# Kernel tuning notes

Measured on AMD Instinct MI355X. Metric: run time of the kernel, lower is better.

Reference implementation:

```python
import jax, jax.numpy as jnp
import numpy as np

B, S, D = 2, 1024, 2048
H, DN, DR, DV, R = 16, 128, 64, 128, 512
E, K, FI, SI = 12, 4, 1408, 2816
THETA = 10000.0
EPS = 1e-6


def rmsnorm(x, w):
    return x * jax.lax.rsqrt(jnp.mean(x * x, -1, keepdims=True) + EPS) * w


def rope(x, cos, sin):
    # interleaved-pair rotation (torch view_as_complex convention)
    x1, x2 = x[..., 0::2], x[..., 1::2]
    return jnp.stack([x1 * cos - x2 * sin, x1 * sin + x2 * cos], axis=-1).reshape(x.shape)


def setup_inputs() -> dict:
    key = jax.random.key(0)
    ks = jax.random.split(key, 16)
    w = lambda k, sh: jax.random.normal(k, sh, jnp.float32) * 0.02
    inp = {
        'x': jax.random.normal(ks[0], (B, S, D), jnp.float32),
        'wq': w(ks[1], (D, H * (DN + DR))),
        'wkv_a': w(ks[2], (D, R + DR)),
        'kv_norm_w': jnp.ones((R,), jnp.float32),
        'wkv_b': w(ks[3], (R, H * (DN + DV))),
        'wo': w(ks[4], (H * DV, D)),
        'norm_w': jnp.ones((D,), jnp.float32),
        'gate_w': w(ks[5], (D, E)),
        'gate_b': jnp.zeros((E,), jnp.float32),
        'w1': w(ks[6], (E, D, FI)),
        'w2': w(ks[7], (E, FI, D)),
        'w3': w(ks[8], (E, D, FI)),
        'ws1': w(ks[9], (D, SI)),
        'ws2': w(ks[10], (SI, D)),
        'ws3': w(ks[11], (D, SI)),
        'mask': jnp.triu(jnp.full((S, S), -1e9, jnp.float32), 1),  # causal
        'start_pos': 0,
    }
    return inp


def reference(x, wq, wkv_a, kv_norm_w, wkv_b, wo, norm_w, gate_w, gate_b,
              w1, w2, w3, ws1, ws2, ws3, mask, start_pos):
    def mla(h):
        q = (h @ wq).reshape(B, S, H, DN + DR)
        q_nope, q_pe = q[..., :DN], q[..., DN:]
        kv = h @ wkv_a                              # [B,S,R+DR]
        kv_lat = rmsnorm(kv[..., :R], kv_norm_w)    # latent KV (kv_lora_rank)
        k_pe = kv[..., R:]                          # [B,S,DR] shared across heads
        kvb = (kv_lat @ wkv_b).reshape(B, S, H, DN + DV)
        k_nope, v = kvb[..., :DN], kvb[..., DN:]
        pos = start_pos + jnp.arange(S)
        inv = 1.0 / (THETA ** (jnp.arange(0, DR, 2, dtype=jnp.float32) / DR))
        ang = pos[:, None].astype(jnp.float32) * inv[None, :]
        cos, sin = jnp.cos(ang), jnp.sin(ang)       # [S, DR//2]
        q_pe = rope(q_pe, cos[None, :, None, :], sin[None, :, None, :])
        k_pe = rope(k_pe, cos[None, :, :], sin[None, :, :])
        scale = (DN + DR) ** -0.5
        scores = (jnp.einsum('bshd,bthd->bhst', q_nope, k_nope)
                  + jnp.einsum('bshd,btd->bhst', q_pe, k_pe)) * scale
        scores = scores + mask[None, None, :, :]
        p = jax.nn.softmax(scores, axis=-1)
        o = jnp.einsum('bhst,bthd->bshd', p, v).reshape(B, S, H * DV)
        return o @ wo

    def moe(h):
        t = h.reshape(-1, D)                        # [T, D]
        T = t.shape[0]
        s = jax.nn.sigmoid(t @ gate_w)              # routing scores [T, E]
        _, topi = jax.lax.top_k(s + gate_b[None, :], K)   # adaptive bias only for selection
        wgt = jnp.take_along_axis(s, topi, axis=1)
        wgt = wgt / jnp.sum(wgt, -1, keepdims=True)
        route = jnp.zeros((T, E), t.dtype).at[jnp.arange(T)[:, None], topi].set(wgt)
        hh = jnp.einsum('td,edi->eti', t, w1)
        gg = jax.nn.silu(hh) * jnp.einsum('td,edi->eti', t, w3)
        eo = jnp.einsum('eti,eid->etd', gg, w2)
        out = jnp.einsum('te,etd->td', route, eo)
        shared = (jax.nn.silu(t @ ws1) * (t @ ws3)) @ ws2
        return (out + shared).reshape(B, S, D)

    first = mla(rmsnorm(x, norm_w)) + x
    return moe(rmsnorm(first, norm_w)) + first
```

## Files before the change

### kernel.cpp

```cpp
#include <hip/hip_runtime.h>
#include <math.h>

typedef unsigned short u16;
typedef __attribute__((ext_vector_type(8))) short short8;
typedef __attribute__((ext_vector_type(8))) _Float16 half8;
typedef __attribute__((ext_vector_type(4))) float f32x4;

__device__ inline u16 f32_to_bf16_rne(float f){
    unsigned int u = __float_as_uint(f);
    unsigned int r = (u + 0x7FFFu + ((u >> 16) & 1u)) >> 16;
    return (u16)r;
}
__device__ inline float bf16_to_f32(u16 h){ return __uint_as_float(((unsigned int)h) << 16); }
__device__ inline u16 h2b(_Float16 h){ union { _Float16 f; u16 u; } x; x.f = h; return x.u; }

__device__ __forceinline__ void glds16(const void* g, void* l){
    __builtin_amdgcn_global_load_lds((const __attribute__((address_space(1))) void*)g,
                                     (__attribute__((address_space(3))) void*)l, 16, 0, 0);
}
#define WAIT_VM0()  { asm volatile("s_waitcnt vmcnt(0)" ::: "memory"); __builtin_amdgcn_sched_barrier(0); }
#define WAIT_VM3()  { asm volatile("s_waitcnt vmcnt(3)" ::: "memory"); __builtin_amdgcn_sched_barrier(0); }
#define WAIT_LGKM0() { asm volatile("s_waitcnt lgkmcnt(0)" ::: "memory"); __builtin_amdgcn_sched_barrier(0); }
#define RAW_BAR()   { __builtin_amdgcn_s_barrier(); __builtin_amdgcn_sched_barrier(0); }

#define TT 2048
#define DD 2048
#define SS 1024
#define NH 16

#define EPI_F32     0
#define EPI_BF16    1
#define EPI_RES     2
#define EPI_SILUMUL 3
#define EPI_F16PAIR 4
#define EPI_QROPE   5
#define EPI_QKV     6

template<int PAIR>
__global__ __launch_bounds__(256) void cvtT_k(const float* __restrict__ W, long long wstr,
        u16* __restrict__ WTh, u16* __restrict__ WTl, long long tstr, int K, int Nsrc){
    __shared__ float L[64][65];
    int e = blockIdx.z;
    const float* Wp = W + (long long)e * wstr;
    int k0 = blockIdx.y * 64, n0 = blockIdx.x * 64;
    int tid = threadIdx.x;
#pragma unroll
    for (int it = 0; it < 4; ++it) {
        int r = (tid >> 4) + it * 16, cc = (tid & 15) * 4;
        int col = n0 + cc;
        float4 v = {0.f, 0.f, 0.f, 0.f};
        if (col + 3 < Nsrc) v = *(const float4*)(Wp + (long long)(k0 + r) * Nsrc + col);
        else {
            const float* p = Wp + (long long)(k0 + r) * Nsrc;
            float tmp[4] = {0.f, 0.f, 0.f, 0.f};
#pragma unroll
            for (int q2 = 0; q2 < 4; q2++) if (col + q2 < Nsrc) tmp[q2] = p[col + q2];
            v.x = tmp[0]; v.y = tmp[1]; v.z = tmp[2]; v.w = tmp[3];
        }
        L[r][cc] = v.x; L[r][cc+1] = v.y; L[r][cc+2] = v.z; L[r][cc+3] = v.w;
    }
    __syncthreads();
#pragma unroll
    for (int it = 0; it < 2; ++it) {
        int idx = it * 256 + tid; int n = idx >> 3, kc = (idx & 7) * 8;
        u16 hi[8], lo[8];
#pragma unroll
        for (int u = 0; u < 8; ++u) {
            float v = L[kc + u][n];
            if (PAIR) { _Float16 h = (_Float16)v; hi[u] = h2b(h); lo[u] = h2b((_Float16)(v - (float)h)); }
            else hi[u] = f32_to_bf16_rne(v);
        }
        long long o = (long long)e * tstr + (long long)(n0 + n) * K + k0 + kc;
        *(short8*)(WTh + o) = *(short8*)hi;
        if (PAIR) *(short8*)(WTl + o) = *(short8*)lo;
    }
}

template<int EPI, bool PREC, bool AGLDS>
__global__ __launch_bounds__(256) void gemm_k(
    const u16* __restrict__ A0, const u16* __restrict__ A1, int lda,
    const u16* __restrict__ BTh, const u16* __restrict__ BTl, long long btstr,
    int M, int N, int K,
    const int* offs, const int* cnt, const int* gather, int ebase,
    void* C0, void* C1, int ldc,
    const void* aux, const float* __restrict__ cosT, const float* __restrict__ sinT,
    int zsplit)
{
    __shared__ u16 AsH[2][4096];
    __shared__ u16 AsL[PREC ? 2 : 1][PREC ? 4096 : 8];
    __shared__ u16 BsH[2][4096];
    __shared__ u16 BsL[PREC ? 2 : 1][PREC ? 4096 : 8];

    int tid  = threadIdx.x;
    int lane = tid & 63;
    int wv   = tid >> 6;
    int wm = (wv >> 1) * 64, wn = (wv & 1) * 64;

    int Lid = blockIdx.y * gridDim.x + blockIdx.x;
    int jj  = Lid >> 3;
    int yb  = jj % gridDim.y;
    int nb  = (Lid & 7) + ((jj / gridDim.y) << 3);
    int n0 = nb * 128;
    if (n0 >= N) return;

    int zz   = blockIdx.z;
    int e    = ebase + ((zsplit > 0 && zz >= zsplit) ? (zz - zsplit) : zz);
    int base = offs ? offs[e] : 0;
    int mc   = cnt ? cnt[e] : M;
    int m0   = yb * 128;
    if (m0 >= mc) return;
    const u16* Bh = BTh + (long long)zz * btstr;
    const u16* Bl = PREC ? (BTl + (long long)zz * btstr) : (const u16*)nullptr;
    void* Cw = (zsplit > 0 && zz >= zsplit) ? C1 : C0;

    int rr_ = tid >> 2, s4 = tid & 3;
    long long arow0 = -1, arow1 = -1;
    if (!AGLDS) {
        if (m0 + rr_ < mc)      arow0 = gather ? (long long)gather[base + m0 + rr_]      : (long long)(base + m0 + rr_);
        if (m0 + rr_ + 64 < mc) arow1 = gather ? (long long)gather[base + m0 + rr_ + 64] : (long long)(base + m0 + rr_ + 64);
    }

    f32x4 acc[4][4];
#pragma unroll
    for (int i = 0; i < 4; i++)
#pragma unroll
        for (int j = 0; j < 4; j++) { f32x4 z = {0.f,0.f,0.f,0.f}; acc[i][j] = z; }

    short8 zer = {0,0,0,0,0,0,0,0};
    short8 a0h = zer, a1h = zer, a0l = zer, a1l = zer;

    int gr0 = wv * 16 + (lane >> 2);
    int gsl = lane & 3;

#define STAGE_GL(PB, KT)                                                         \
    {                                                                            \
        _Pragma("unroll")                                                        \
        for (int it = 0; it < 2; ++it) {                                         \
            int r = it * 64 + gr0;                                               \
            int s = gsl ^ ((r >> 1) & 3);                                        \
            glds16(Bh + (long long)(n0 + r) * K + (KT) + s * 8,                  \
                   (char*)&BsH[PB][0] + it * 4096 + wv * 1024);                  \
            if (PREC)                                                            \
                glds16(Bl + (long long)(n0 + r) * K + (KT) + s * 8,              \
                       (char*)&BsL[PB][0] + it * 4096 + wv * 1024);              \
            if (AGLDS) {                                                         \
                glds16(A0 + (long long)(base + m0 + r) * lda + (KT) + s * 8,     \
                       (char*)&AsH[PB][0] + it * 4096 + wv * 1024);              \
                if (PREC)                                                        \
                    glds16(A1 + (long long)(base + m0 + r) * lda + (KT) + s * 8, \
                           (char*)&AsL[PB][0] + it * 4096 + wv * 1024);          \
            }                                                                    \
        }                                                                        \
        if (!AGLDS) {                                                            \
            a0h = (arow0 >= 0) ? *(const short8*)(A0 + arow0 * lda + (KT) + s4 * 8) : zer; \
            a1h = (arow1 >= 0) ? *(const short8*)(A0 + arow1 * lda + (KT) + s4 * 8) : zer; \
            if (PREC) {                                                          \
                a0l = (arow0 >= 0) ? *(const short8*)(A1 + arow0 * lda + (KT) + s4 * 8) : zer; \
                a1l = (arow1 >= 0) ? *(const short8*)(A1 + arow1 * lda + (KT) + s4 * 8) : zer; \
            }                                                                    \
        }                                                                        \
    }

    int pb = 0;
    STAGE_GL(0, 0);
    for (int kt = 0; kt < K; kt += 32) {
        WAIT_VM0();
        if (!AGLDS) {
            int d0 = rr_ * 64 + 16 * (s4 ^ ((rr_ >> 1) & 3));
            int r1w = rr_ + 64;
            int d1 = r1w * 64 + 16 * (s4 ^ ((r1w >> 1) & 3));
            *(short8*)((char*)&AsH[pb][0] + d0) = a0h;
            *(short8*)((char*)&AsH[pb][0] + d1) = a1h;
            if (PREC) {
                *(short8*)((char*)&AsL[pb][0] + d0) = a0l;
                *(short8*)((char*)&AsL[pb][0] + d1) = a1l;
            }
            WAIT_LGKM0();
        }
        RAW_BAR();
        if (kt + 32 < K) { STAGE_GL(pb ^ 1, kt + 32); }
        if (PREC) {
            half8 ah[4], al[4];
#pragma unroll
            for (int i = 0; i < 4; i++) {
                int ra = wm + i * 16 + (lane & 15);
                int off = ra * 64 + 16 * ((lane >> 4) ^ ((ra >> 1) & 3));
                ah[i] = *(const half8*)((const char*)&AsH[pb][0] + off);
                al[i] = *(const half8*)((const char*)&AsL[pb][0] + off);
            }
#pragma unroll
            for (int j = 0; j < 4; j++) {
                int rb = wn + j * 16 + (lane & 15);
                int off = rb * 64 + 16 * ((lane >> 4) ^ ((rb >> 1) & 3));
                half8 bh = *(const half8*)((const char*)&BsH[pb][0] + off);
                half8 bl = *(const half8*)((const char*)&BsL[pb][0] + off);
#pragma unroll
                for (int i = 0; i < 4; i++) {
                    acc[i][j] = __builtin_amdgcn_mfma_f32_16x16x32_f16(ah[i], bh, acc[i][j], 0, 0, 0);
                    acc[i][j] = __builtin_amdgcn_mfma_f32_16x16x32_f16(ah[i], bl, acc[i][j], 0, 0, 0);
                    acc[i][j] = __builtin_amdgcn_mfma_f32_16x16x32_f16(al[i], bh, acc[i][j], 0, 0, 0);
                }
            }
        } else {
            short8 af[4];
#pragma unroll
            for (int i = 0; i < 4; i++) {
                int ra = wm + i * 16 + (lane & 15);
                af[i] = *(const short8*)((const char*)&AsH[pb][0] + ra * 64 + 16 * ((lane >> 4) ^ ((ra >> 1) & 3)));
            }
#pragma unroll
            for (int j = 0; j < 4; j++) {
                int rb = wn + j * 16 + (lane & 15);
                short8 bfr = *(const short8*)((const char*)&BsH[pb][0] + rb * 64 + 16 * ((lane >> 4) ^ ((rb >> 1) & 3)));
#pragma unroll
                for (int i = 0; i < 4; i++)
                    acc[i][j] = __builtin_amdgcn_mfma_f32_16x16x32_bf16(af[i], bfr, acc[i][j], 0, 0, 0);
            }
        }
        pb ^= 1;
    }
#undef STAGE_GL

    if (EPI == EPI_QROPE || (EPI == EPI_QKV && n0 < 3072)) {
#pragma unroll
        for (int i = 0; i < 4; i++) {
            int rr0 = m0 + wm + i * 16 + ((lane >> 4) << 2);
#pragma unroll
            for (int j = 0; j < 4; j++) {
                int col = n0 + wn + j * 16 + (lane & 15);
                int hd = col % 192;
#pragma unroll
                for (int r = 0; r < 4; r++) {
                    int rr = rr0 + r;
                    float v = acc[i][j][r];
                    float pv = __shfl_xor(v, 1);
                    float outv = v;
                    if (hd >= 128) {
                        int s = rr & (SS - 1);
                        int pi2 = (hd - 128) >> 1;
                        float cc_ = cosT[s * 32 + pi2], sn_ = sinT[s * 32 + pi2];
                        bool odd = col & 1;
                        float a0 = odd ? pv : v, a1 = odd ? v : pv;
                        outv = odd ? (a0 * sn_ + a1 * cc_) : (a0 * cc_ - a1 * sn_);
                    }
                    long long cidx = (long long)rr * ldc + col;
                    _Float16 hh = (_Float16)outv;
                    ((u16*)C0)[cidx] = h2b(hh);
                    ((u16*)C1)[cidx] = h2b((_Float16)(outv - (float)hh));
                }
            }
        }
    } else if (EPI == EPI_QKV) {
        float* kvo = (float*)aux;
#pragma unroll
        for (int i = 0; i < 4; i++) {
            int rr0 = m0 + wm + i * 16 + ((lane >> 4) << 2);
#pragma unroll
            for (int j = 0; j < 4; j++) {
                int col = n0 + wn + j * 16 + (lane & 15);
                if (col >= 3648) continue;
#pragma unroll
                for (int r = 0; r < 4; r++) {
                    int rr = rr0 + r;
                    kvo[(long long)rr * 576 + (col - 3072)] = acc[i][j][r];
                }
            }
        }
    } else {
#pragma unroll
        for (int i = 0; i < 4; i++) {
            int rbase = m0 + wm + i * 16 + ((lane >> 4) << 2);
#pragma unroll
            for (int j = 0; j < 4; j++) {
                int col = n0 + wn + j * 16 + (lane & 15);
                if (col >= N) continue;
#pragma unroll
                for (int r = 0; r < 4; r++) {
                    int rr = rbase + r;
                    if (rr >= mc) continue;
                    long long cidx = (long long)(base + rr) * ldc + col;
                    float v = acc[i][j][r];
                    if (EPI == EPI_F32)      ((float*)C0)[cidx] = v;
                    else if (EPI == EPI_BF16) ((u16*)Cw)[cidx] = f32_to_bf16_rne(v);
                    else if (EPI == EPI_RES)  ((float*)C0)[cidx] = v + ((const float*)aux)[cidx];
                    else if (EPI == EPI_SILUMUL) {
                        float h1v = bf16_to_f32(((const u16*)aux)[cidx]);
                        float g = h1v / (1.f + __expf(-h1v)) * v;
                        ((u16*)C0)[cidx] = f32_to_bf16_rne(g);
                    } else {
                        _Float16 hh = (_Float16)v;
                        ((u16*)C0)[cidx] = h2b(hh);
                        ((u16*)C1)[cidx] = h2b((_Float16)(v - (float)hh));
                    }
                }
            }
        }
    }
}

template<int EPI, bool GATHER>
__global__ __launch_bounds__(256) void gemm3_k(
    const u16* __restrict__ A0, int lda,
    const u16* __restrict__ BTh, long long btstr,
    int M, int N, int K,
    const int* offs, const int* cnt, const int* gather, int ebase,
    void* C0, void* C1, int ldc,
    const void* aux, int zsplit)
{
    __shared__ u16 As[3][2048];
    __shared__ u16 Bs[3][4096];

    int tid  = threadIdx.x;
    int lane = tid & 63;
    int wv   = tid >> 6;
    int wm = (wv >> 1) * 32, wn = (wv & 1) * 64;

    int Lid = blockIdx.y * gridDim.x + blockIdx.x;
    int jj  = Lid >> 3;
    int yb  = jj % gridDim.y;
    int nb  = (Lid & 7) + ((jj / gridDim.y) << 3);
    int n0 = nb * 128;
    if (n0 >= N) return;

    int zz   = blockIdx.z;
    int e    = ebase + ((zsplit > 0 && zz >= zsplit) ? (zz - zsplit) : zz);
    int base = offs ? offs[e] : 0;
    int mc   = cnt ? cnt[e] : M;
    int m0   = yb * 64;
    if (m0 >= mc) return;
    const u16* Bh = BTh + (long long)zz * btstr;
    void* Cw = (zsplit > 0 && zz >= zsplit) ? C1 : C0;

    int rr = tid >> 2;
    int sl4 = tid & 3;
    int sA = sl4 ^ ((rr >> 1) & 3);
    long long bro0, bro1, aro0;
    {
        int rb1 = rr + 64;
        int sB1 = sl4 ^ ((rb1 >> 1) & 3);
        bro0 = (long long)(n0 + rr) * K + sA * 8;
        bro1 = (long long)(n0 + rb1) * K + sB1 * 8;
        int ar = m0 + rr; ar = (ar < mc) ? ar : (mc - 1);
        long long ga = GATHER ? (long long)gather[base + ar] : (long long)(base + ar);
        aro0 = ga * (long long)lda + sA * 8;
    }

    f32x4 acc[2][4];
#pragma unroll
    for (int i = 0; i < 2; i++)
#pragma unroll
        for (int j = 0; j < 4; j++) { f32x4 z = {0.f,0.f,0.f,0.f}; acc[i][j] = z; }

#define STG3(PB, KT)                                                        \
    {                                                                       \
        glds16(Bh + bro0 + (KT), (char*)&Bs[PB][0] + wv * 1024);            \
        glds16(Bh + bro1 + (KT), (char*)&Bs[PB][0] + 4096 + wv * 1024);     \
        glds16(A0 + aro0 + (KT), (char*)&As[PB][0] + wv * 1024);            \
    }

    int nst = K >> 5;
    STG3(0, 0);
    if (nst > 1) STG3(1, 32);
    for (int t = 0; t < nst; ++t) {
        if (t + 1 < nst) { WAIT_VM3(); }
        else            { WAIT_VM0(); }
        RAW_BAR();
        if (t + 2 < nst) { int p2 = (t + 2) % 3; STG3(p2, (t + 2) * 32); }
        int pb = t % 3;
        short8 af[2];
#pragma unroll
        for (int i = 0; i < 2; i++) {
            int ra = wm + i * 16 + (lane & 15);
            af[i] = *(const short8*)((const char*)&As[pb][0] + ra * 64 + 16 * ((lane >> 4) ^ ((ra >> 1) & 3)));
        }
#pragma unroll
        for (int j = 0; j < 4; j++) {
            int rb = wn + j * 16 + (lane & 15);
            short8 bfr = *(const short8*)((const char*)&Bs[pb][0] + rb * 64 + 16 * ((lane >> 4) ^ ((rb >> 1) & 3)));
#pragma unroll
            for (int i = 0; i < 2; i++)
                acc[i][j] = __builtin_amdgcn_mfma_f32_16x16x32_bf16(af[i], bfr, acc[i][j], 0, 0, 0);
        }
    }
#undef STG3

#pragma unroll
    for (int i = 0; i < 2; i++) {
        int rbase = m0 + wm + i * 16 + ((lane >> 4) << 2);
#pragma unroll
        for (int j = 0; j < 4; j++) {
            int col = n0 + wn + j * 16 + (lane & 15);
            if (col >= N) continue;
#pragma unroll
            for (int r = 0; r < 4; r++) {
                int rr2 = rbase + r;
                if (rr2 >= mc) continue;
                long long cidx = (long long)(base + rr2) * ldc + col;
                float v = acc[i][j][r];
                if (EPI == EPI_BF16) ((u16*)Cw)[cidx] = f32_to_bf16_rne(v);
                else {
                    float h1v = bf16_to_f32(((const u16*)aux)[cidx]);
                    float g = h1v / (1.f + __expf(-h1v)) * v;
                    ((u16*)C0)[cidx] = f32_to_bf16_rne(g);
                }
            }
        }
    }
}

__global__ __launch_bounds__(256) void silumul_k(u16* __restrict__ g, const u16* __restrict__ h3,
                                                 long long n){
    long long i = ((long long)blockIdx.x * 256 + threadIdx.x) * 8;
    if (i >= n) return;
    short8 a = *(const short8*)(g + i);
    short8 b = *(const short8*)(h3 + i);
    u16 o[8];
#pragma unroll
    for (int u = 0; u < 8; ++u) {
        float x = bf16_to_f32((u16)a[u]);
        float y = bf16_to_f32((u16)b[u]);
        o[u] = f32_to_bf16_rne(x / (1.f + __expf(-x)) * y);
    }
    *(short8*)(g + i) = *(short8*)o;
}

__global__ void costab_k(const int* sp, float* ct, float* st){
    int idx = blockIdx.x * 256 + threadIdx.x;
    if (idx >= SS * 32) return;
    int i = idx & 31, s = idx >> 5;
    float inv = powf(10000.0f, -(float)i / 32.0f);
    float a = (float)(sp[0] + s) * inv;
    ct[idx] = cosf(a);
    st[idx] = sinf(a);
}

template<int MODE>
__global__ __launch_bounds__(256) void rms_k(const float* __restrict__ x, const float* __restrict__ w,
                                             u16* o0, u16* o1){
    int t = blockIdx.x, tid = threadIdx.x;
    const float* row = x + (long long)t * DD;
    float4 v0 = *(const float4*)(row + tid * 4);
    float4 v1 = *(const float4*)(row + 1024 + tid * 4);
    float ss = v0.x*v0.x + v0.y*v0.y + v0.z*v0.z + v0.w*v0.w
             + v1.x*v1.x + v1.y*v1.y + v1.z*v1.z + v1.w*v1.w;
#pragma unroll
    for (int d = 1; d < 64; d <<= 1) ss += __shfl_xor(ss, d, 64);
    __shared__ float red[4];
    if ((tid & 63) == 0) red[tid >> 6] = ss;
    __syncthreads();
    float sc = rsqrtf((red[0] + red[1] + red[2] + red[3]) / (float)DD + 1e-6f);
    float a[8];
    a[0]=v0.x; a[1]=v0.y; a[2]=v0.z; a[3]=v0.w; a[4]=v1.x; a[5]=v1.y; a[6]=v1.z; a[7]=v1.w;
#pragma unroll
    for (int q2 = 0; q2 < 8; q2++) {
        int d = (q2 < 4) ? (tid * 4 + q2) : (1024 + tid * 4 + (q2 - 4));
        float y = a[q2] * sc * w[d];
        if (MODE == 0) {
            _Float16 hh = (_Float16)y;
            o0[(long long)t * DD + d] = h2b(hh);
            o1[(long long)t * DD + d] = h2b((_Float16)(y - (float)hh));
        } else {
            o0[(long long)t * DD + d] = f32_to_bf16_rne(y);
        }
    }
}

__global__ __launch_bounds__(256) void kvprep_k(const float* __restrict__ kv, const float* __restrict__ kw,
    const float* __restrict__ ct, const float* __restrict__ st,
    u16* lath, u16* latl, u16* kpeh, u16* kpel){
    int t = blockIdx.x, tid = threadIdx.x;
    const float* row = kv + (long long)t * 576;
    float x0 = row[tid], x1 = row[256 + tid];
    float ss = x0 * x0 + x1 * x1;
#pragma unroll
    for (int d = 1; d < 64; d <<= 1) ss += __shfl_xor(ss, d, 64);
    __shared__ float red[4];
    if ((tid & 63) == 0) red[tid >> 6] = ss;
    __syncthreads();
    float sc = rsqrtf((red[0] + red[1] + red[2] + red[3]) / 512.f + 1e-6f);
    float y0 = x0 * sc * kw[tid], y1 = x1 * sc * kw[256 + tid];
    _Float16 h0 = (_Float16)y0, h1 = (_Float16)y1;
    lath[(long long)t * 512 + tid] = h2b(h0);
    latl[(long long)t * 512 + tid] = h2b((_Float16)(y0 - (float)h0));
    lath[(long long)t * 512 + 256 + tid] = h2b(h1);
    latl[(long long)t * 512 + 256 + tid] = h2b((_Float16)(y1 - (float)h1));
    if (tid < 32) {
        int s = t & (SS - 1);
        float a0 = row[512 + 2 * tid], a1 = row[513 + 2 * tid];
        float c = ct[s * 32 + tid], sn = st[s * 32 + tid];
        float r0 = a0 * c - a1 * sn, r1 = a0 * sn + a1 * c;
        _Float16 p0 = (_Float16)r0, p1 = (_Float16)r1;
        kpeh[(long long)t * 64 + 2 * tid]     = h2b(p0);
        kpel[(long long)t * 64 + 2 * tid]     = h2b((_Float16)(r0 - (float)p0));
        kpeh[(long long)t * 64 + 2 * tid + 1] = h2b(p1);
        kpel[(long long)t * 64 + 2 * tid + 1] = h2b((_Float16)(r1 - (float)p1));
    }
}

__global__ __launch_bounds__(256) void vtprep_k(const u16* __restrict__ kvbh, const u16* __restrict__ kvbl,
                                                u16* vth, u16* vtl){
    __shared__ u16 L[64][136];
    int bh = blockIdx.x, st = blockIdx.y, pl = blockIdx.z;
    const u16* src = pl ? kvbl : kvbh;
    u16* dst = pl ? vtl : vth;
    int b = bh >> 4, hh = bh & 15;
    int tid = threadIdx.x;
#pragma unroll
    for (int it = 0; it < 4; ++it) {
        int idx = it * 256 + tid; int sl = idx >> 4, dc = idx & 15;
        long long t = (long long)b * SS + st * 64 + sl;
        *(short8*)&L[sl][dc * 8] = *(const short8*)(src + t * 4096 + hh * 256 + 128 + dc * 8);
    }
    __syncthreads();
#pragma unroll
    for (int it = 0; it < 4; ++it) {
        int idx = it * 256 + tid; int d = idx >> 3, sc = idx & 7;
        short8 v;
#pragma unroll
        for (int u = 0; u < 8; u++) v[u] = (short)L[sc * 8 + u][d];
        *(short8*)(dst + ((long long)bh * 128 + d) * SS + st * 64 + sc * 8) = v;
    }
}

__global__ __launch_bounds__(256) void attn_k(
    const u16* __restrict__ qh_, const u16* __restrict__ ql_,
    const u16* __restrict__ kvbh, const u16* __restrict__ kvbl,
    const u16* __restrict__ kpeh, const u16* __restrict__ kpel,
    const u16* __restrict__ vth, const u16* __restrict__ vtl,
    u16* ohi, u16* olo)
{
    __shared__ u16 KsH[32][200], KsL[32][200];
    __shared__ u16 VsH[128][40], VsL[128][40];
    __shared__ u16 PlH[4][16][40], PlL[4][16][40];
    int bx = blockIdx.x, bh = blockIdx.y;
    int qi = (bh & 16) ? bx : (15 - bx);
    int b = bh >> 4, h = bh & 15;
    int tid = threadIdx.x, lane = tid & 63, wv = tid >> 6;
    int q0 = qi * 64;
    const u16* vbh = vth + (long long)bh * 128 * SS;
    const u16* vbl = vtl + (long long)bh * 128 * SS;

    half8 qh[6], ql[6];
    {
        int row = q0 + wv * 16 + (lane & 15);
        const u16* ph = qh_ + (long long)(b * SS + row) * 3072 + h * 192 + (lane >> 4) * 8;
        const u16* pl = ql_ + (long long)(b * SS + row) * 3072 + h * 192 + (lane >> 4) * 8;
#pragma unroll
        for (int ks = 0; ks < 6; ks++) {
            qh[ks] = *(const half8*)(ph + ks * 32);
            ql[ks] = *(const half8*)(pl + ks * 32);
        }
    }
    float mrun[4], lrun[4];
    f32x4 oacc[8];
#pragma unroll
    for (int r = 0; r < 4; r++) { mrun[r] = -1e30f; lrun[r] = 0.f; }
#pragma unroll
    for (int f = 0; f < 8; f++) { f32x4 z = {0.f,0.f,0.f,0.f}; oacc[f] = z; }
    const float scale = 0.07216878364870322f;

    short8 kh0, kh1, kh2, kl0, kl1, kl2, vh0, vh1, vl0, vl1;
    int kr0 = tid / 24 + 0,  kc0 = tid % 24;
    int kr1 = (256 + tid) / 24, kc1 = (256 + tid) % 24;
    int kr2 = (512 + tid) / 24, kc2 = (512 + tid) % 24;
    int vr0 = tid >> 2, vc0 = tid & 3;
    int vr1 = (256 + tid) >> 2, vc1 = vc0;

#define ALOAD(T0)                                                                   \
    {                                                                               \
        long long tg0 = (long long)b * SS + (T0);                                   \
        if (kc0 < 16) { kh0 = *(const short8*)(kvbh + (tg0 + kr0) * 4096 + h * 256 + kc0 * 8); \
                        kl0 = *(const short8*)(kvbl + (tg0 + kr0) * 4096 + h * 256 + kc0 * 8); } \
        else          { kh0 = *(const short8*)(kpeh + (tg0 + kr0) * 64 + (kc0 - 16) * 8);      \
                        kl0 = *(const short8*)(kpel + (tg0 + kr0) * 64 + (kc0 - 16) * 8); }    \
        if (kc1 < 16) { kh1 = *(const short8*)(kvbh + (tg0 + kr1) * 4096 + h * 256 + kc1 * 8); \
                        kl1 = *(const short8*)(kvbl + (tg0 + kr1) * 4096 + h * 256 + kc1 * 8); } \
        else          { kh1 = *(const short8*)(kpeh + (tg0 + kr1) * 64 + (kc1 - 16) * 8);      \
                        kl1 = *(const short8*)(kpel + (tg0 + kr1) * 64 + (kc1 - 16) * 8); }    \
        if (kc2 < 16) { kh2 = *(const short8*)(kvbh + (tg0 + kr2) * 4096 + h * 256 + kc2 * 8); \
                        kl2 = *(const short8*)(kvbl + (tg0 + kr2) * 4096 + h * 256 + kc2 * 8); } \
        else          { kh2 = *(const short8*)(kpeh + (tg0 + kr2) * 64 + (kc2 - 16) * 8);      \
                        kl2 = *(const short8*)(kpel + (tg0 + kr2) * 64 + (kc2 - 16) * 8); }    \
        vh0 = *(const short8*)(vbh + (long long)vr0 * SS + (T0) + vc0 * 8);         \
        vl0 = *(const short8*)(vbl + (long long)vr0 * SS + (T0) + vc0 * 8);         \
        vh1 = *(const short8*)(vbh + (long long)vr1 * SS + (T0) + vc1 * 8);         \
        vl1 = *(const short8*)(vbl + (long long)vr1 * SS + (T0) + vc1 * 8);         \
    }

    int ntile = 2 * qi + 2;
    ALOAD(0);
    for (int ti = 0; ti < ntile; ++ti) {
        int t0 = ti * 32;
        WAIT_VM0();
        RAW_BAR();
        *(short8*)&KsH[kr0][kc0 * 8] = kh0; *(short8*)&KsL[kr0][kc0 * 8] = kl0;
        *(short8*)&KsH[kr1][kc1 * 8] = kh1; *(short8*)&KsL[kr1][kc1 * 8] = kl1;
        *(short8*)&KsH[kr2][kc2 * 8] = kh2; *(short8*)&KsL[kr2][kc2 * 8] = kl2;
        *(short8*)&VsH[vr0][vc0 * 8] = vh0; *(short8*)&VsL[vr0][vc0 * 8] = vl0;
        *(short8*)&VsH[vr1][vc1 * 8] = vh1; *(short8*)&VsL[vr1][vc1 * 8] = vl1;
        WAIT_LGKM0();
        RAW_BAR();
        if (ti + 1 < ntile) ALOAD(t0 + 32);
        f32x4 s[2];
#pragma unroll
        for (int nt = 0; nt < 2; ++nt) {
            f32x4 a = {0.f,0.f,0.f,0.f};
#pragma unroll
            for (int ks = 0; ks < 6; ++ks) {
                half8 kh = *(const half8*)&KsH[nt * 16 + (lane & 15)][ks * 32 + (lane >> 4) * 8];
                half8 kl = *(const half8*)&KsL[nt * 16 + (lane & 15)][ks * 32 + (lane >> 4) * 8];
                a = __builtin_amdgcn_mfma_f32_16x16x32_f16(qh[ks], kh, a, 0, 0, 0);
                a = __builtin_amdgcn_mfma_f32_16x16x32_f16(qh[ks], kl, a, 0, 0, 0);
                a = __builtin_amdgcn_mfma_f32_16x16x32_f16(ql[ks], kh, a, 0, 0, 0);
            }
            s[nt] = a;
        }
#pragma unroll
        for (int nt = 0; nt < 2; ++nt)
#pragma unroll
            for (int r = 0; r < 4; ++r) {
                float v = s[nt][r] * scale;
                if (ti >= 2 * qi) {
                    int t = t0 + nt * 16 + (lane & 15);
                    int sq = q0 + wv * 16 + (lane >> 4) * 4 + r;
                    if (t > sq) v = -1e30f;
                }
                s[nt][r] = v;
            }
        float corr[4];
#pragma unroll
        for (int r = 0; r < 4; ++r) {
            float m = fmaxf(s[0][r], s[1][r]);
#pragma unroll
            for (int d = 1; d < 16; d <<= 1) m = fmaxf(m, __shfl_xor(m, d, 64));
            float mn = fmaxf(mrun[r], m);
            corr[r] = __expf(mrun[r] - mn);
            mrun[r] = mn;
        }
        float rs[4] = {0.f, 0.f, 0.f, 0.f};
#pragma unroll
        for (int nt = 0; nt < 2; ++nt)
#pragma unroll
            for (int r = 0; r < 4; ++r) {
                float p = __expf(s[nt][r] - mrun[r]);
                s[nt][r] = p;
                rs[r] += p;
            }
#pragma unroll
        for (int r = 0; r < 4; ++r) {
            float tsum = rs[r];
#pragma unroll
            for (int d = 1; d < 16; d <<= 1) tsum += __shfl_xor(tsum, d, 64);
            lrun[r] = lrun[r] * corr[r] + tsum;
        }
#pragma unroll
        for (int f = 0; f < 8; f++)
#pragma unroll
            for (int r = 0; r < 4; r++) oacc[f][r] *= corr[r];
#pragma unroll
        for (int nt = 0; nt < 2; ++nt)
#pragma unroll
            for (int r = 0; r < 4; ++r) {
                float p = s[nt][r];
                _Float16 ph = (_Float16)p;
                PlH[wv][(lane >> 4) * 4 + r][nt * 16 + (lane & 15)] = h2b(ph);
                PlL[wv][(lane >> 4) * 4 + r][nt * 16 + (lane & 15)] = h2b((_Float16)(p - (float)ph));
            }
        half8 pfh = *(const half8*)&PlH[wv][lane & 15][(lane >> 4) * 8];
        half8 pfl = *(const half8*)&PlL[wv][lane & 15][(lane >> 4) * 8];
#pragma unroll
        for (int f = 0; f < 8; ++f) {
            half8 vh = *(const half8*)&VsH[f * 16 + (lane & 15)][(lane >> 4) * 8];
            half8 vl = *(const half8*)&VsL[f * 16 + (lane & 15)][(lane >> 4) * 8];
            oacc[f] = __builtin_amdgcn_mfma_f32_16x16x32_f16(pfh, vh, oacc[f], 0, 0, 0);
            oacc[f] = __builtin_amdgcn_mfma_f32_16x16x32_f16(pfh, vl, oacc[f], 0, 0, 0);
            oacc[f] = __builtin_amdgcn_mfma_f32_16x16x32_f16(pfl, vh, oacc[f], 0, 0, 0);
        }
    }
#undef ALOAD
#pragma unroll
    for (int f = 0; f < 8; ++f)
#pragma unroll
        for (int r = 0; r < 4; ++r) {
            int sq = q0 + wv * 16 + (lane >> 4) * 4 + r;
            float v = oacc[f][r] / lrun[r];
            _Float16 hh = (_Float16)v;
            long long o = ((long long)(b * SS + sq)) * 2048 + h * 128 + f * 16 + (lane & 15);
            ohi[o] = h2b(hh);
            olo[o] = h2b((_Float16)(v - (float)hh));
        }
}

__global__ __launch_bounds__(256) void gate_k(const float* __restrict__ first,
    const float* __restrict__ nw, const float* __restrict__ gw, const float* __restrict__ gb,
    int* topi, float* wgt){
    int wv = threadIdx.x >> 6, lane = threadIdx.x & 63;
    int t = blockIdx.x * 4 + wv;
    const float* row = first + (long long)t * DD;
    float rv[32];
    float ss = 0.f;
#pragma unroll
    for (int it = 0; it < 32; ++it) {
        float v = row[it * 64 + lane];
        rv[it] = v;
        ss += v * v;
    }
#pragma unroll
    for (int d = 1; d < 64; d <<= 1) ss += __shfl_xor(ss, d, 64);
    float sc = rsqrtf(ss / (float)DD + 1e-6f);
    float acc[12];
#pragma unroll
    for (int e = 0; e < 12; e++) acc[e] = 0.f;
#pragma unroll
    for (int it = 0; it < 32; ++it) {
        int i = it * 64 + lane;
        float v = rv[it] * sc * nw[i];
        const float* g = gw + (long long)i * 12;
        float4 g0 = *(const float4*)g;
        float4 g1 = *(const float4*)(g + 4);
        float4 g2 = *(const float4*)(g + 8);
        acc[0] += v * g0.x; acc[1] += v * g0.y; acc[2]  += v * g0.z; acc[3]  += v * g0.w;
        acc[4] += v * g1.x; acc[5] += v * g1.y; acc[6]  += v * g1.z; acc[7]  += v * g1.w;
        acc[8] += v * g2.x; acc[9] += v * g2.y; acc[10] += v * g2.z; acc[11] += v * g2.w;
    }
#pragma unroll
    for (int e = 0; e < 12; e++)
#pragma unroll
        for (int d = 1; d < 64; d <<= 1) acc[e] += __shfl_xor(acc[e], d, 64);
    if (lane == 0) {
        float s[12], rank[12];
#pragma unroll
        for (int e = 0; e < 12; e++) { s[e] = 1.f / (1.f + expf(-acc[e])); rank[e] = s[e] + gb[e]; }
        int sel[4]; float wv4[4]; float wsum = 0.f;
#pragma unroll
        for (int k = 0; k < 4; k++) {
            int bi = 0; float bv = -1e30f;
#pragma unroll
            for (int e = 0; e < 12; e++) if (rank[e] > bv) { bv = rank[e]; bi = e; }
            sel[k] = bi; rank[bi] = -1e31f;
            wv4[k] = s[bi]; wsum += s[bi];
        }
#pragma unroll
        for (int k = 0; k < 4; k++) {
            topi[t * 4 + k] = sel[k];
            wgt[t * 4 + k] = wv4[k] / wsum;
        }
    }
}

__global__ __launch_bounds__(256) void offs_k(const int* __restrict__ topi,
                                              int* cnt, int* offs, int* cur){
    __shared__ int lh[4][12];
    int tid = threadIdx.x, wv = tid >> 6, lane = tid & 63;
    int c[12];
#pragma unroll
    for (int e = 0; e < 12; e++) c[e] = 0;
    for (int i = tid; i < TT * 4; i += 256) {
        int e = topi[i];
#pragma unroll
        for (int q = 0; q < 12; q++) c[q] += (e == q) ? 1 : 0;
    }
#pragma unroll
    for (int e = 0; e < 12; e++) {
        int v = c[e];
#pragma unroll
        for (int d = 1; d < 64; d <<= 1) v += __shfl_xor(v, d, 64);
        if (lane == 0) lh[wv][e] = v;
    }
    __syncthreads();
    if (tid == 0) {
        int a = 0;
        for (int e = 0; e < 12; e++) {
            int tot = lh[0][e] + lh[1][e] + lh[2][e] + lh[3][e];
            cnt[e] = tot; offs[e] = a; a += tot; cur[e] = 0;
        }
        offs[12] = a;
    }
}

__global__ __launch_bounds__(256) void scatter_k(const int* __restrict__ topi,
    const float* __restrict__ wgt, const int* __restrict__ offs,
    int* cur, int* tok, float* wgl, int* posm){
    __shared__ int lh[12];
    __shared__ int gb[12];
    int tid = threadIdx.x;
    if (tid < 12) lh[tid] = 0;
    __syncthreads();
    int t = blockIdx.x * 256 + tid;
    int e4[4], lr[4];
#pragma unroll
    for (int k = 0; k < 4; k++) {
        e4[k] = topi[t * 4 + k];
        lr[k] = atomicAdd(&lh[e4[k]], 1);
    }
    __syncthreads();
    if (tid < 12) gb[tid] = atomicAdd(&cur[tid], lh[tid]);
    __syncthreads();
#pragma unroll
    for (int k = 0; k < 4; k++) {
        int pos = offs[e4[k]] + gb[e4[k]] + lr[k];
        tok[pos] = t;
        wgl[pos] = wgt[t * 4 + k];
        posm[t * 4 + k] = pos;
    }
}

__global__ void final_k(const float* __restrict__ first, const u16* __restrict__ so,
    const u16* __restrict__ eo, const int* __restrict__ posm, const float* __restrict__ wgl,
    float* out){
    int idx = blockIdx.x * 256 + threadIdx.x;
    int d4 = idx & 511, t = idx >> 9;
    int d = d4 * 4;
    const float* fp = first + (long long)t * DD + d;
    const u16* sp = so + (long long)t * DD + d;
    float r0 = fp[0] + bf16_to_f32(sp[0]);
    float r1 = fp[1] + bf16_to_f32(sp[1]);
    float r2 = fp[2] + bf16_to_f32(sp[2]);
    float r3 = fp[3] + bf16_to_f32(sp[3]);
#pragma unroll
    for (int k = 0; k < 4; k++) {
        int pos = posm[t * 4 + k];
        float wv = wgl[pos];
        const u16* ep = eo + (long long)pos * DD + d;
        r0 += wv * bf16_to_f32(ep[0]);
        r1 += wv * bf16_to_f32(ep[1]);
        r2 += wv * bf16_to_f32(ep[2]);
        r3 += wv * bf16_to_f32(ep[3]);
    }
    float4 res = {r0, r1, r2, r3};
    *(float4*)(out + (long long)t * DD + d) = res;
}

extern "C" void kernel_launch(void* const* d_in, const int* in_sizes, int n_in,
                              void* d_out, int out_size, void* d_ws, size_t ws_size,
                              hipStream_t stream)
{
    const float* x       = (const float*)d_in[0];
    const float* wq      = (const float*)d_in[1];
    const float* wkv_a   = (const float*)d_in[2];
    const float* kvnw    = (const float*)d_in[3];
    const float* wkv_b   = (const float*)d_in[4];
    const float* wo      = (const float*)d_in[5];
    const float* norm_w  = (const float*)d_in[6];
    const float* gate_w  = (const float*)d_in[7];
    const float* gate_b  = (const float*)d_in[8];
    const float* w1      = (const float*)d_in[9];
    const float* w2      = (const float*)d_in[10];
    const float* w3      = (const float*)d_in[11];
    const float* ws1     = (const float*)d_in[12];
    const float* ws2     = (const float*)d_in[13];
    const float* ws3     = (const float*)d_in[14];
    const int*   startp  = (const int*)d_in[16];
    char* ws = (char*)d_ws;

    const size_t O_COS = 0, O_SIN = 131072, O_KPEH = 262144, O_KPEL = 524288;
    const size_t O_TOPI = 786432, O_WGT = 819200, O_TOK = 851968, O_WGL = 884736, O_POSM = 917504;
    const size_t O_CNT = 950272, O_OFFS = 950336, O_CUR = 950400;
    const size_t O_WB = 1048576;
    const size_t B2 = 31457280;
    const size_t O_H    = B2,             O_HLO  = B2 + 8388608;
    const size_t O_Q    = B2 + 16777216,  O_QLO  = B2 + 29360128;
    const size_t O_KVF  = B2 + 41943040;
    const size_t O_LATH = B2 + 46661632,  O_LATL = B2 + 48758784;
    const size_t O_KVBH = B2 + 50855936,  O_KVBL = B2 + 67633152;
    const size_t O_VTH  = B2,             O_VTL  = B2 + 8388608;
    const size_t O_OH   = B2 + 84410368,  O_OL   = B2 + 92798976;
    const size_t O_FIRST= B2 + 16777216;
    const size_t O_TBF  = B2;
    const size_t O_H1   = B2 + 33554432;
    const size_t O_EO   = B2 + 56623104;
    const size_t O_SH1  = B2 + 90177536;
    const size_t O_SO   = B2 + 101711872;

    float* cosT = (float*)(ws + O_COS);  float* sinT = (float*)(ws + O_SIN);
    u16* kpeh = (u16*)(ws + O_KPEH);     u16* kpel = (u16*)(ws + O_KPEL);
    int* topi = (int*)(ws + O_TOPI);     float* wgt = (float*)(ws + O_WGT);
    int* tok = (int*)(ws + O_TOK);       float* wgl = (float*)(ws + O_WGL);
    int* posm = (int*)(ws + O_POSM);
    int* cntp = (int*)(ws + O_CNT); int* offsp = (int*)(ws + O_OFFS); int* curp = (int*)(ws + O_CUR);
    u16* WB   = (u16*)(ws + O_WB);
    u16* hhi = (u16*)(ws + O_H);    u16* hlo = (u16*)(ws + O_HLO);
    u16* qhp = (u16*)(ws + O_Q);    u16* qlp = (u16*)(ws + O_QLO);
    float* kvf = (float*)(ws + O_KVF);
    u16* lath = (u16*)(ws + O_LATH); u16* latl = (u16*)(ws + O_LATL);
    u16* kvbh = (u16*)(ws + O_KVBH); u16* kvbl = (u16*)(ws + O_KVBL);
    u16* vth = (u16*)(ws + O_VTH);  u16* vtl = (u16*)(ws + O_VTL);
    u16* oh  = (u16*)(ws + O_OH);   u16* ol  = (u16*)(ws + O_OL);
    float* first = (float*)(ws + O_FIRST);
    u16* tbf = (u16*)(ws + O_TBF);
    u16* h1buf = (u16*)(ws + O_H1); u16* eo = (u16*)(ws + O_EO);
    u16* sh1 = (u16*)(ws + O_SH1);  u16* sobuf = (u16*)(ws + O_SO);
    u16* sh3 = (u16*)(ws + O_H1);

    costab_k<<<128, 256, 0, stream>>>(startp, cosT, sinT);
    rms_k<0><<<TT, 256, 0, stream>>>(x, norm_w, hhi, hlo);

    cvtT_k<1><<<dim3(48, 32, 1), 256, 0, stream>>>(wq, 0, WB, WB + 7602176, 0, 2048, 3072);
    cvtT_k<1><<<dim3(10, 32, 1), 256, 0, stream>>>(wkv_a, 0, WB + 6291456, WB + 13893632, 0, 2048, 576);
    gemm_k<EPI_QKV, true, true><<<dim3(32, 16, 1), 256, 0, stream>>>(
        hhi, hlo, 2048, WB, WB + 7602176, 0, 2048, 3712, 2048,
        nullptr, nullptr, nullptr, 0, qhp, qlp, 3072, kvf, cosT, sinT, 0);
    kvprep_k<<<TT, 256, 0, stream>>>(kvf, kvnw, cosT, sinT, lath, latl, kpeh, kpel);

    cvtT_k<1><<<dim3(64, 8, 1), 256, 0, stream>>>(wkv_b, 0, WB, WB + 2097152, 0, 512, 4096);
    gemm_k<EPI_F16PAIR, true, true><<<dim3(32, 16, 1), 256, 0, stream>>>(
        lath, latl, 512, WB, WB + 2097152, 0, 2048, 4096, 512,
        nullptr, nullptr, nullptr, 0, kvbh, kvbl, 4096, nullptr, nullptr, nullptr, 0);

    vtprep_k<<<dim3(32, 16, 2), 256, 0, stream>>>(kvbh, kvbl, vth, vtl);
    attn_k<<<dim3(16, 32, 1), 256, 0, stream>>>(qhp, qlp, kvbh, kvbl, kpeh, kpel, vth, vtl, oh, ol);

    cvtT_k<1><<<dim3(32, 32, 1), 256, 0, stream>>>(wo, 0, WB, WB + 4194304, 0, 2048, 2048);
    gemm_k<EPI_RES, true, true><<<dim3(16, 16, 1), 256, 0, stream>>>(
        oh, ol, 2048, WB, WB + 4194304, 0, 2048, 2048, 2048,
        nullptr, nullptr, nullptr, 0, first, nullptr, 2048, x, nullptr, nullptr, 0);

    rms_k<1><<<TT, 256, 0, stream>>>(first, norm_w, tbf, nullptr);
    gate_k<<<512, 256, 0, stream>>>(first, norm_w, gate_w, gate_b, topi, wgt);
    offs_k<<<1, 256, 0, stream>>>(topi, cntp, offsp, curp);
    scatter_k<<<8, 256, 0, stream>>>(topi, wgt, offsp, curp, tok, wgl, posm);

    const long long SW = (long long)2816 * 2048;
    cvtT_k<0><<<dim3(44, 32, 1), 256, 0, stream>>>(ws1, 0, WB, nullptr, 0, 2048, 2816);
    cvtT_k<0><<<dim3(44, 32, 1), 256, 0, stream>>>(ws3, 0, WB + SW, nullptr, 0, 2048, 2816);
    gemm3_k<EPI_BF16, false><<<dim3(24, 32, 2), 256, 0, stream>>>(
        tbf, 2048, WB, SW, 2048, 2816, 2048,
        nullptr, nullptr, nullptr, 0, sh1, sh3, 2816, nullptr, 1);
    silumul_k<<<2816, 256, 0, stream>>>(sh1, sh3, (long long)2048 * 2816);
    cvtT_k<0><<<dim3(32, 44, 1), 256, 0, stream>>>(ws2, 0, WB, nullptr, 0, 2816, 2048);
    gemm3_k<EPI_BF16, false><<<dim3(16, 32, 1), 256, 0, stream>>>(
        sh1, 2816, WB, 0, 2048, 2048, 2816,
        nullptr, nullptr, nullptr, 0, sobuf, nullptr, 2048, nullptr, 0);

    const long long EW = (long long)2048 * 1408;
    for (int g = 0; g < 3; ++g) {
        cvtT_k<0><<<dim3(22, 32, 4), 256, 0, stream>>>(w1 + (long long)g * 4 * EW, EW, WB, nullptr, EW, 2048, 1408);
        gemm3_k<EPI_BF16, true><<<dim3(16, 32, 4), 256, 0, stream>>>(
            tbf, 2048, WB, EW, 2048, 1408, 2048,
            offsp, cntp, tok, 4 * g, h1buf, nullptr, 1408, nullptr, 0);
        cvtT_k<0><<<dim3(22, 32, 4), 256, 0, stream>>>(w3 + (long long)g * 4 * EW, EW, WB, nullptr, EW, 2048, 1408);
        gemm3_k<EPI_SILUMUL, true><<<dim3(16, 32, 4), 256, 0, stream>>>(
            tbf, 2048, WB, EW, 2048, 1408, 2048,
            offsp, cntp, tok, 4 * g, h1buf, nullptr, 1408, h1buf, 0);
        cvtT_k<0><<<dim3(32, 22, 4), 256, 0, stream>>>(w2 + (long long)g * 4 * EW, EW, WB, nullptr, EW, 1408, 2048);
        gemm3_k<EPI_BF16, false><<<dim3(16, 32, 4), 256, 0, stream>>>(
            h1buf, 1408, WB, EW, 2048, 2048, 1408,
            offsp, cntp, nullptr, 4 * g, eo, nullptr, 2048, nullptr, 0);
    }

    final_k<<<4096, 256, 0, stream>>>(first, sobuf, eo, posm, wgl, (float*)d_out);
}
```

Before: 1.178 ms.

## Use triple-buffered 64x128 tile GEMM for split-precision attention projections

```diff
diff --git a/kernel.cpp b/kernel.cpp
--- a/kernel.cpp
+++ b/kernel.cpp
@@ -20,6 +20,7 @@
 }
 #define WAIT_VM0()  { asm volatile("s_waitcnt vmcnt(0)" ::: "memory"); __builtin_amdgcn_sched_barrier(0); }
 #define WAIT_VM3()  { asm volatile("s_waitcnt vmcnt(3)" ::: "memory"); __builtin_amdgcn_sched_barrier(0); }
+#define WAIT_VM6()  { asm volatile("s_waitcnt vmcnt(6)" ::: "memory"); __builtin_amdgcn_sched_barrier(0); }
 #define WAIT_LGKM0() { asm volatile("s_waitcnt lgkmcnt(0)" ::: "memory"); __builtin_amdgcn_sched_barrier(0); }
 #define RAW_BAR()   { __builtin_amdgcn_s_barrier(); __builtin_amdgcn_sched_barrier(0); }
 
@@ -76,25 +77,23 @@
     }
 }
 
-template<int EPI, bool PREC, bool AGLDS>
-__global__ __launch_bounds__(256) void gemm_k(
+template<int EPI>
+__global__ __launch_bounds__(256) void gemmp3_k(
     const u16* __restrict__ A0, const u16* __restrict__ A1, int lda,
-    const u16* __restrict__ BTh, const u16* __restrict__ BTl, long long btstr,
+    const u16* __restrict__ BTh, const u16* __restrict__ BTl,
     int M, int N, int K,
-    const int* offs, const int* cnt, const int* gather, int ebase,
-    void* C0, void* C1, int ldc,
-    const void* aux, const float* __restrict__ cosT, const float* __restrict__ sinT,
-    int zsplit)
+    void* C0, void* C1, int ldc, const void* aux,
+    const float* __restrict__ cosT, const float* __restrict__ sinT)
 {
-    __shared__ u16 AsH[2][4096];
-    __shared__ u16 AsL[PREC ? 2 : 1][PREC ? 4096 : 8];
-    __shared__ u16 BsH[2][4096];
-    __shared__ u16 BsL[PREC ? 2 : 1][PREC ? 4096 : 8];
+    __shared__ u16 AsH[3][2048];
+    __shared__ u16 AsL[3][2048];
+    __shared__ u16 BsH[3][4096];
+    __shared__ u16 BsL[3][4096];
 
     int tid  = threadIdx.x;
     int lane = tid & 63;
     int wv   = tid >> 6;
-    int wm = (wv >> 1) * 64, wn = (wv & 1) * 64;
+    int wm = (wv >> 1) * 32, wn = (wv & 1) * 64;
 
     int Lid = blockIdx.y * gridDim.x + blockIdx.x;
     int jj  = Lid >> 3;
@@ -102,128 +101,86 @@
     int nb  = (Lid & 7) + ((jj / gridDim.y) << 3);
     int n0 = nb * 128;
     if (n0 >= N) return;
-
-    int zz   = blockIdx.z;
-    int e    = ebase + ((zsplit > 0 && zz >= zsplit) ? (zz - zsplit) : zz);
-    int base = offs ? offs[e] : 0;
-    int mc   = cnt ? cnt[e] : M;
-    int m0   = yb * 128;
-    if (m0 >= mc) return;
-    const u16* Bh = BTh + (long long)zz * btstr;
-    const u16* Bl = PREC ? (BTl + (long long)zz * btstr) : (const u16*)nullptr;
-    void* Cw = (zsplit > 0 && zz >= zsplit) ? C1 : C0;
-
-    int rr_ = tid >> 2, s4 = tid & 3;
-    long long arow0 = -1, arow1 = -1;
-    if (!AGLDS) {
-        if (m0 + rr_ < mc)      arow0 = gather ? (long long)gather[base + m0 + rr_]      : (long long)(base + m0 + rr_);
-        if (m0 + rr_ + 64 < mc) arow1 = gather ? (long long)gather[base + m0 + rr_ + 64] : (long long)(base + m0 + rr_ + 64);
-    }
-
-    f32x4 acc[4][4];
-#pragma unroll
-    for (int i = 0; i < 4; i++)
+    int m0 = yb * 64;
+    if (m0 >= M) return;
+
+    int rr = tid >> 2;
+    int sl4 = tid & 3;
+    int sA = sl4 ^ ((rr >> 1) & 3);
+    int rb1 = rr + 64;
+    int sB1 = sl4 ^ ((rb1 >> 1) & 3);
+    long long aro = (long long)(m0 + rr) * lda + sA * 8;
+    long long bro0 = (long long)(n0 + rr) * K + sA * 8;
+    long long bro1 = (long long)(n0 + rb1) * K + sB1 * 8;
+
+    f32x4 acc[2][4];
+#pragma unroll
+    for (int i = 0; i < 2; i++)
 #pragma unroll
         for (int j = 0; j < 4; j++) { f32x4 z = {0.f,0.f,0.f,0.f}; acc[i][j] = z; }
 
-    short8 zer = {0,0,0,0,0,0,0,0};
-    short8 a0h = zer, a1h = zer, a0l = zer, a1l = zer;
-
-    int gr0 = wv * 16 + (lane >> 2);
-    int gsl = lane & 3;
-
-#define STAGE_GL(PB, KT)                                                         \
-    {                                                                            \
-        _Pragma("unroll")                                                        \
-        for (int it = 0; it < 2; ++it) {                                         \
-            int r = it * 64 + gr0;                                               \
-            int s = gsl ^ ((r >> 1) & 3);                                        \
-            glds16(Bh + (long long)(n0 + r) * K + (KT) + s * 8,                  \
-                   (char*)&BsH[PB][0] + it * 4096 + wv * 1024);                  \
-            if (PREC)                                                            \
-                glds16(Bl + (long long)(n0 + r) * K + (KT) + s * 8,              \
-                       (char*)&BsL[PB][0] + it * 4096 + wv * 1024);              \
-            if (AGLDS) {                                                         \
-                glds16(A0 + (long long)(base + m0 + r) * lda + (KT) + s * 8,     \
-                       (char*)&AsH[PB][0] + it * 4096 + wv * 1024);              \
-                if (PREC)                                                        \
-                    glds16(A1 + (long long)(base + m0 + r) * lda + (KT) + s * 8, \
-                           (char*)&AsL[PB][0] + it * 4096 + wv * 1024);          \
-            }                                                                    \
-        }                                                                        \
-        if (!AGLDS) {                                                            \
-            a0h = (arow0 >= 0) ? *(const short8*)(A0 + arow0 * lda + (KT) + s4 * 8) : zer; \
-            a1h = (arow1 >= 0) ? *(const short8*)(A0 + arow1 * lda + (KT) + s4 * 8) : zer; \
-            if (PREC) {                                                          \
-                a0l = (arow0 >= 0) ? *(const short8*)(A1 + arow0 * lda + (KT) + s4 * 8) : zer; \
-                a1l = (arow1 >= 0) ? *(const short8*)(A1 + arow1 * lda + (KT) + s4 * 8) : zer; \
-            }                                                                    \
-        }                                                                        \
-    }
-
-    int pb = 0;
-    STAGE_GL(0, 0);
-    for (int kt = 0; kt < K; kt += 32) {
-        WAIT_VM0();
-        if (!AGLDS) {
-            int d0 = rr_ * 64 + 16 * (s4 ^ ((rr_ >> 1) & 3));
-            int r1w = rr_ + 64;
-            int d1 = r1w * 64 + 16 * (s4 ^ ((r1w >> 1) & 3));
-            *(short8*)((char*)&AsH[pb][0] + d0) = a0h;
-            *(short8*)((char*)&AsH[pb][0] + d1) = a1h;
-            if (PREC) {
-                *(short8*)((char*)&AsL[pb][0] + d0) = a0l;
-                *(short8*)((char*)&AsL[pb][0] + d1) = a1l;
+#define STGP(PB, KT)                                                        \
+    {                                                                       \
+        glds16(BTh + bro0 + (KT), (char*)&BsH[PB][0] + wv * 1024);          \
+        glds16(BTh + bro1 + (KT), (char*)&BsH[PB][0] + 4096 + wv * 1024);   \
+        glds16(BTl + bro0 + (KT), (char*)&BsL[PB][0] + wv * 1024);          \
+        glds16(BTl + bro1 + (KT), (char*)&BsL[PB][0] + 4096 + wv * 1024);   \
+        glds16(A0 + aro + (KT),  (char*)&AsH[PB][0] + wv * 1024);           \
+        glds16(A1 + aro + (KT),  (char*)&AsL[PB][0] + wv * 1024);           \
+    }
+
+    int nst = K >> 5;
+    STGP(0, 0);
+    if (nst > 1) STGP(1, 32);
+    for (int t = 0; t < nst; ++t) {
+        if (t + 1 < nst) { WAIT_VM6(); }
+        else            { WAIT_VM0(); }
+        RAW_BAR();
+        if (t + 2 < nst) { int p2 = (t + 2) % 3; STGP(p2, (t + 2) * 32); }
+        int pb = t % 3;
+        half8 ah[2], al[2];
+#pragma unroll
+        for (int i = 0; i < 2; i++) {
+            int ra = wm + i * 16 + (lane & 15);
+            int off = ra * 64 + 16 * ((lane >> 4) ^ ((ra >> 1) & 3));
+            ah[i] = *(const half8*)((const char*)&AsH[pb][0] + off);
+            al[i] = *(const half8*)((const char*)&AsL[pb][0] + off);
+        }
+#pragma unroll
+        for (int j = 0; j < 4; j++) {
+            int rb = wn + j * 16 + (lane & 15);
+            int off = rb * 64 + 16 * ((lane >> 4) ^ ((rb >> 1) & 3));
+            half8 bh = *(const half8*)((const char*)&BsH[pb][0] + off);
+            half8 bl = *(const half8*)((const char*)&BsL[pb][0] + off);
+#pragma unroll
+            for (int i = 0; i < 2; i++) {
+                acc[i][j] = __builtin_amdgcn_mfma_f32_16x16x32_f16(ah[i], bh, acc[i][j], 0, 0, 0);
+                acc[i][j] = __builtin_amdgcn_mfma_f32_16x16x32_f16(ah[i], bl, acc[i][j], 0, 0, 0);
+                acc[i][j] = __builtin_amdgcn_mfma_f32_16x16x32_f16(al[i], bh, acc[i][j], 0, 0, 0);
             }
-            WAIT_LGKM0();
-        }
-        RAW_BAR();
-        if (kt + 32 < K) { STAGE_GL(pb ^ 1, kt + 32); }
-        if (PREC) {
-            half8 ah[4], al[4];
-#pragma unroll
-            for (int i = 0; i < 4; i++) {
-                int ra = wm + i * 16 + (lane & 15);
-                int off = ra * 64 + 16 * ((lane >> 4) ^ ((ra >> 1) & 3));
-                ah[i] = *(const half8*)((const char*)&AsH[pb][0] + off);
-                al[i] = *(const half8*)((const char*)&AsL[pb][0] + off);
-            }
+        }
+    }
+#undef STGP
+
+    if (EPI == EPI_QKV && n0 >= 3072) {
+        float* kvo = (float*)aux;
+#pragma unroll
+        for (int i = 0; i < 2; i++) {
+            int rr0 = m0 + wm + i * 16 + ((lane >> 4) << 2);
 #pragma unroll
             for (int j = 0; j < 4; j++) {
-                int rb = wn + j * 16 + (lane & 15);
-                int off = rb * 64 + 16 * ((lane >> 4) ^ ((rb >> 1) & 3));
-                half8 bh = *(const half8*)((const char*)&BsH[pb][0] + off);
-                half8 bl = *(const half8*)((const char*)&BsL[pb][0] + off);
-#pragma unroll
-                for (int i = 0; i < 4; i++) {
-                    acc[i][j] = __builtin_amdgcn_mfma_f32_16x16x32_f16(ah[i], bh, acc[i][j], 0, 0, 0);
-                    acc[i][j] = __builtin_amdgcn_mfma_f32_16x16x32_f16(ah[i], bl, acc[i][j], 0, 0, 0);
-                    acc[i][j] = __builtin_amdgcn_mfma_f32_16x16x32_f16(al[i], bh, acc[i][j], 0, 0, 0);
+                int col = n0 + wn + j * 16 + (lane & 15);
+                if (col >= 3648) continue;
+#pragma unroll
+                for (int r = 0; r < 4; r++) {
+                    int rr2 = rr0 + r;
+                    kvo[(long long)rr2 * 576 + (col - 3072)] = acc[i][j][r];
                 }
             }
-        } else {
-            short8 af[4];
-#pragma unroll
-            for (int i = 0; i < 4; i++) {
-                int ra = wm + i * 16 + (lane & 15);
-                af[i] = *(const short8*)((const char*)&AsH[pb][0] + ra * 64 + 16 * ((lane >> 4) ^ ((ra >> 1) & 3)));
-            }
-#pragma unroll
-            for (int j = 0; j < 4; j++) {
-                int rb = wn + j * 16 + (lane & 15);
-                short8 bfr = *(const short8*)((const char*)&BsH[pb][0] + rb * 64 + 16 * ((lane >> 4) ^ ((rb >> 1) & 3)));
-#pragma unroll
-                for (int i = 0; i < 4; i++)
-                    acc[i][j] = __builtin_amdgcn_mfma_f32_16x16x32_bf16(af[i], bfr, acc[i][j], 0, 0, 0);
-            }
-        }
-        pb ^= 1;
-    }
-#undef STAGE_GL
-
-    if (EPI == EPI_QROPE || (EPI == EPI_QKV && n0 < 3072)) {
-#pragma unroll
-        for (int i = 0; i < 4; i++) {
+        }
+    } else if (EPI == EPI_QKV) {
+#pragma unroll
+        for (int i = 0; i < 2; i++) {
             int rr0 = m0 + wm + i * 16 + ((lane >> 4) << 2);
 #pragma unroll
             for (int j = 0; j < 4; j++) {
@@ -231,62 +188,40 @@
                 int hd = col % 192;
 #pragma unroll
                 for (int r = 0; r < 4; r++) {
-                    int rr = rr0 + r;
+                    int rr2 = rr0 + r;
                     float v = acc[i][j][r];
                     float pv = __shfl_xor(v, 1);
                     float outv = v;
                     if (hd >= 128) {
-                        int s = rr & (SS - 1);
+                        int s = rr2 & (SS - 1);
                         int pi2 = (hd - 128) >> 1;
                         float cc_ = cosT[s * 32 + pi2], sn_ = sinT[s * 32 + pi2];
                         bool odd = col & 1;
                         float a0 = odd ? pv : v, a1 = odd ? v : pv;
                         outv = odd ? (a0 * sn_ + a1 * cc_) : (a0 * cc_ - a1 * sn_);
                     }
-                    long long cidx = (long long)rr * ldc + col;
+                    long long cidx = (long long)rr2 * ldc + col;
                     _Float16 hh = (_Float16)outv;
                     ((u16*)C0)[cidx] = h2b(hh);
                     ((u16*)C1)[cidx] = h2b((_Float16)(outv - (float)hh));
                 }
             }
         }
-    } else if (EPI == EPI_QKV) {
-        float* kvo = (float*)aux;
-#pragma unroll
-        for (int i = 0; i < 4; i++) {
+    } else {
+#pragma unroll
+        for (int i = 0; i < 2; i++) {
             int rr0 = m0 + wm + i * 16 + ((lane >> 4) << 2);
-#pragma unroll
-            for (int j = 0; j < 4; j++) {
-                int col = n0 + wn + j * 16 + (lane & 15);
-                if (col >= 3648) continue;
-#pragma unroll
-                for (int r = 0; r < 4; r++) {
-                    int rr = rr0 + r;
-                    kvo[(long long)rr * 576 + (col - 3072)] = acc[i][j][r];
-                }
-            }
-        }
-    } else {
-#pragma unroll
-        for (int i = 0; i < 4; i++) {
-            int rbase = m0 + wm + i * 16 + ((lane >> 4) << 2);
 #pragma unroll
             for (int j = 0; j < 4; j++) {
                 int col = n0 + wn + j * 16 + (lane & 15);
                 if (col >= N) continue;
 #pragma unroll
                 for (int r = 0; r < 4; r++) {
-                    int rr = rbase + r;
-                    if (rr >= mc) continue;
-                    long long cidx = (long long)(base + rr) * ldc + col;
+                    int rr2 = rr0 + r;
+                    long long cidx = (long long)rr2 * ldc + col;
                     float v = acc[i][j][r];
-                    if (EPI == EPI_F32)      ((float*)C0)[cidx] = v;
-                    else if (EPI == EPI_BF16) ((u16*)Cw)[cidx] = f32_to_bf16_rne(v);
-                    else if (EPI == EPI_RES)  ((float*)C0)[cidx] = v + ((const float*)aux)[cidx];
-                    else if (EPI == EPI_SILUMUL) {
-                        float h1v = bf16_to_f32(((const u16*)aux)[cidx]);
-                        float g = h1v / (1.f + __expf(-h1v)) * v;
-                        ((u16*)C0)[cidx] = f32_to_bf16_rne(g);
+                    if (EPI == EPI_RES) {
+                        ((float*)C0)[cidx] = v + ((const float*)aux)[cidx];
                     } else {
                         _Float16 hh = (_Float16)v;
                         ((u16*)C0)[cidx] = h2b(hh);
@@ -897,23 +832,23 @@
 
     cvtT_k<1><<<dim3(48, 32, 1), 256, 0, stream>>>(wq, 0, WB, WB + 7602176, 0, 2048, 3072);
     cvtT_k<1><<<dim3(10, 32, 1), 256, 0, stream>>>(wkv_a, 0, WB + 6291456, WB + 13893632, 0, 2048, 576);
-    gemm_k<EPI_QKV, true, true><<<dim3(32, 16, 1), 256, 0, stream>>>(
-        hhi, hlo, 2048, WB, WB + 7602176, 0, 2048, 3712, 2048,
-        nullptr, nullptr, nullptr, 0, qhp, qlp, 3072, kvf, cosT, sinT, 0);
+    gemmp3_k<EPI_QKV><<<dim3(32, 32, 1), 256, 0, stream>>>(
+        hhi, hlo, 2048, WB, WB + 7602176, 2048, 3712, 2048,
+        qhp, qlp, 3072, kvf, cosT, sinT);
     kvprep_k<<<TT, 256, 0, stream>>>(kvf, kvnw, cosT, sinT, lath, latl, kpeh, kpel);
 
     cvtT_k<1><<<dim3(64, 8, 1), 256, 0, stream>>>(wkv_b, 0, WB, WB + 2097152, 0, 512, 4096);
-    gemm_k<EPI_F16PAIR, true, true><<<dim3(32, 16, 1), 256, 0, stream>>>(
-        lath, latl, 512, WB, WB + 2097152, 0, 2048, 4096, 512,
-        nullptr, nullptr, nullptr, 0, kvbh, kvbl, 4096, nullptr, nullptr, nullptr, 0);
+    gemmp3_k<EPI_F16PAIR><<<dim3(32, 32, 1), 256, 0, stream>>>(
+        lath, latl, 512, WB, WB + 2097152, 2048, 4096, 512,
+        kvbh, kvbl, 4096, nullptr, nullptr, nullptr);
 
     vtprep_k<<<dim3(32, 16, 2), 256, 0, stream>>>(kvbh, kvbl, vth, vtl);
     attn_k<<<dim3(16, 32, 1), 256, 0, stream>>>(qhp, qlp, kvbh, kvbl, kpeh, kpel, vth, vtl, oh, ol);
 
     cvtT_k<1><<<dim3(32, 32, 1), 256, 0, stream>>>(wo, 0, WB, WB + 4194304, 0, 2048, 2048);
-    gemm_k<EPI_RES, true, true><<<dim3(16, 16, 1), 256, 0, stream>>>(
-        oh, ol, 2048, WB, WB + 4194304, 0, 2048, 2048, 2048,
-        nullptr, nullptr, nullptr, 0, first, nullptr, 2048, x, nullptr, nullptr, 0);
+    gemmp3_k<EPI_RES><<<dim3(16, 32, 1), 256, 0, stream>>>(
+        oh, ol, 2048, WB, WB + 4194304, 2048, 2048, 2048,
+        first, nullptr, 2048, x, nullptr, nullptr);
 
     rms_k<1><<<TT, 256, 0, stream>>>(first, norm_w, tbf, nullptr);
     gate_k<<<512, 256, 0, stream>>>(first, norm_w, gate_w, gate_b, topi, wgt);
```

New measurement: 1.202 ms. No clear change (+2.0%).
